# Kernel tuning notes

Hardware: AMD Instinct MI355X
Metric: run time of the kernel (lower is better)

## Reference

```python
import jax, jax.numpy as jnp
import numpy as np

N_NODES = 100000
N_EDGES = 800000
D_IN = 512
D_OUT = 512


def setup_inputs() -> dict:
    key = jax.random.key(0)
    ks = jax.random.split(key, 6)
    std = 1.0 / np.sqrt(D_OUT)
    return {
        "x": jax.random.normal(ks[0], (N_NODES, D_IN), dtype=jnp.float32),
        "adj_row": jax.random.randint(ks[1], (N_EDGES,), 0, N_NODES, dtype=jnp.int32),
        "adj_col": jax.random.randint(ks[2], (N_EDGES,), 0, N_NODES, dtype=jnp.int32),
        "adj_vals": jax.random.uniform(ks[3], (N_EDGES,), dtype=jnp.float32),
        "weight": jax.random.uniform(ks[4], (D_IN, D_OUT), minval=-std, maxval=std, dtype=jnp.float32),
        "b": jax.random.uniform(ks[5], (D_OUT,), minval=-std, maxval=std, dtype=jnp.float32),
    }


def reference(x, adj_row, adj_col, adj_vals, weight, b):
    # support = X W  : dense GEMM [N, D_in] x [D_in, D_out]
    support = jnp.matmul(x, weight)
    # output = A @ support + b, A given as COO (row, col, vals)
    gathered = adj_vals[:, None] * support[adj_col]  # [E, D_out]
    out = jax.ops.segment_sum(gathered, adj_row, num_segments=N_NODES)
    return out + b
```

## Files before the change

### kernel.cpp

```cpp
#include <hip/hip_runtime.h>
#include <hip/hip_bf16.h>
#include <stdint.h>

#define D 512
#define D4 (D / 4)

typedef __bf16 bf16x8 __attribute__((ext_vector_type(8)));
typedef float  f32x4  __attribute__((ext_vector_type(4)));

__device__ __forceinline__ unsigned short f2bf(float f) {
    uint32_t u = __float_as_uint(f);
    uint32_t r = u + 0x7fffu + ((u >> 16) & 1u);
    return (unsigned short)(r >> 16);
}

__device__ __forceinline__ uint32_t pack2(float lo, float hi) {
    return (uint32_t)f2bf(lo) | ((uint32_t)f2bf(hi) << 16);
}

__global__ __launch_bounds__(256) void cvt_x_kernel(const float4* __restrict__ x,
                                                    uint4* __restrict__ xb,
                                                    long n8) {
    long i = (long)blockIdx.x * 256 + threadIdx.x;
    if (i >= n8) return;
    float4 a = x[i * 2];
    float4 b = x[i * 2 + 1];
    uint4 o;
    o.x = pack2(a.x, a.y);
    o.y = pack2(a.z, a.w);
    o.z = pack2(b.x, b.y);
    o.w = pack2(b.z, b.w);
    xb[i] = o;
}

__global__ __launch_bounds__(256) void cvt_w_kernel(const float* __restrict__ w,
                                                    unsigned short* __restrict__ wt) {
    __shared__ float t[32][33];
    const int tx = threadIdx.x & 31;
    const int ty = threadIdx.x >> 5;
    const int n0 = blockIdx.x * 32;
    const int k0 = blockIdx.y * 32;
#pragma unroll
    for (int i = 0; i < 4; ++i)
        t[ty + i * 8][tx] = w[(long)(k0 + ty + i * 8) * D + n0 + tx];
    __syncthreads();
#pragma unroll
    for (int i = 0; i < 4; ++i)
        wt[(long)(n0 + ty + i * 8) * D + k0 + tx] = f2bf(t[tx][ty + i * 8]);
}

__global__ __launch_bounds__(256) void zero_kernel(int* __restrict__ p, int n) {
    int i = blockIdx.x * 256 + threadIdx.x;
    if (i < n) p[i] = 0;
}

__global__ __launch_bounds__(256) void hist_kernel(const int* __restrict__ erow,
                                                   int* __restrict__ cnt, int nE) {
    int i = blockIdx.x * 256 + threadIdx.x;
    int stride = gridDim.x * 256;
    for (; i < nE; i += stride) atomicAdd(&cnt[erow[i]], 1);
}

__global__ __launch_bounds__(1024) void scan_kernel(const int* __restrict__ cnt,
                                                    int* __restrict__ rowptr,
                                                    int* __restrict__ heads,
                                                    int M) {
    __shared__ int wsum[16];
    __shared__ int wpre[16];
    __shared__ int s_carry;
    const int lane = threadIdx.x & 63;
    const int wv   = threadIdx.x >> 6;
    if (threadIdx.x == 0) s_carry = 0;
    __syncthreads();
    for (int base = 0; base < M; base += 1024) {
        const int i = base + (int)threadIdx.x;
        const int v = (i < M) ? cnt[i] : 0;
        int s = v;
#pragma unroll
        for (int off = 1; off < 64; off <<= 1) {
            int t = __shfl_up(s, off);
            if (lane >= off) s += t;
        }
        if (lane == 63) wsum[wv] = s;
        __syncthreads();
        if (threadIdx.x == 0) {
            int acc = s_carry;
#pragma unroll
            for (int j = 0; j < 16; ++j) { wpre[j] = acc; acc += wsum[j]; }
            s_carry = acc;
        }
        __syncthreads();
        const int excl = wpre[wv] + s - v;
        if (i < M) { rowptr[i] = excl; heads[i] = excl; }
        __syncthreads();
    }
    if (threadIdx.x == 0) rowptr[M] = s_carry;
}

__global__ __launch_bounds__(256) void edge_sort_kernel(const int* __restrict__ erow,
                                                        const int* __restrict__ ecol,
                                                        const float* __restrict__ eval,
                                                        int* __restrict__ heads,
                                                        int* __restrict__ scol,
                                                        float* __restrict__ sval,
                                                        int nE) {
    int i = blockIdx.x * 256 + threadIdx.x;
    int stride = gridDim.x * 256;
    for (; i < nE; i += stride) {
        const int r = erow[i];
        const int p = atomicAdd(&heads[r], 1);
        scol[p] = ecol[i];
        sval[p] = eval[i];
    }
}

__global__ __launch_bounds__(256) void gemm_kernel(const unsigned short* __restrict__ Xb,
                                                   const unsigned short* __restrict__ Wt,
                                                   unsigned short* __restrict__ Sup,
                                                   int M) {
    __shared__ __align__(16) unsigned short As[128 * 64];
    __shared__ __align__(16) unsigned short Bs[128 * 64];
    const int tid  = threadIdx.x;
    const int wv   = tid >> 6;
    const int lane = tid & 63;
    const int tileM = blockIdx.x * 128;
    const int tileN = blockIdx.y * 128;
    const int wm = wv >> 1, wn = wv & 1;

    f32x4 acc[4][4];
#pragma unroll
    for (int i = 0; i < 4; ++i)
#pragma unroll
        for (int j = 0; j < 4; ++j) acc[i][j] = (f32x4)0.0f;

    const int srow = lane >> 3;
    const int sgrn = (lane & 7) ^ srow;
    const int scol = sgrn * 8;

    const int fm  = lane & 15;
    const int fkq = lane >> 4;

    for (int kt = 0; kt < D; kt += 64) {
        __syncthreads();
#pragma unroll
        for (int i = 0; i < 4; ++i) {
            const int c   = wv * 4 + i;
            const int row = c * 8 + srow;
            int rg = tileM + row;
            rg = (rg < M) ? rg : (M - 1);
            const unsigned short* ga = Xb + (long)rg * D + kt + scol;
            __builtin_amdgcn_global_load_lds(
                (const __attribute__((address_space(1))) void*)ga,
                (__attribute__((address_space(3))) void*)(As + c * 512), 16, 0, 0);
            const unsigned short* gb = Wt + (long)(tileN + row) * D + kt + scol;
            __builtin_amdgcn_global_load_lds(
                (const __attribute__((address_space(1))) void*)gb,
                (__attribute__((address_space(3))) void*)(Bs + c * 512), 16, 0, 0);
        }
        __syncthreads();
#pragma unroll
        for (int kk = 0; kk < 2; ++kk) {
            bf16x8 af[4], bfr[4];
#pragma unroll
            for (int mi = 0; mi < 4; ++mi) {
                const int m = wm * 64 + mi * 16 + fm;
                const int g = (kk * 4 + fkq) ^ (m & 7);
                af[mi] = *(const bf16x8*)(As + m * 64 + g * 8);
            }
#pragma unroll
            for (int ni = 0; ni < 4; ++ni) {
                const int n = wn * 64 + ni * 16 + fm;
                const int g = (kk * 4 + fkq) ^ (n & 7);
                bfr[ni] = *(const bf16x8*)(Bs + n * 64 + g * 8);
            }
#pragma unroll
            for (int mi = 0; mi < 4; ++mi)
#pragma unroll
                for (int ni = 0; ni < 4; ++ni)
                    acc[mi][ni] = __builtin_amdgcn_mfma_f32_16x16x32_bf16(
                        af[mi], bfr[ni], acc[mi][ni], 0, 0, 0);
        }
    }

    const int colb = tileN + wn * 64 + fm;
#pragma unroll
    for (int mi = 0; mi < 4; ++mi) {
        const int rb = tileM + wm * 64 + mi * 16 + fkq * 4;
#pragma unroll
        for (int r = 0; r < 4; ++r) {
            const int row = rb + r;
            if (row < M) {
                unsigned short* dst = Sup + (long)row * D + colb;
#pragma unroll
                for (int ni = 0; ni < 4; ++ni)
                    dst[ni * 16] = f2bf(acc[mi][ni][r]);
            }
        }
    }
}

__global__ __launch_bounds__(256) void aggregate_kernel(const unsigned short* __restrict__ sup,
                                                        const int* __restrict__ rowptr,
                                                        const int* __restrict__ scol,
                                                        const float* __restrict__ sval,
                                                        const float* __restrict__ bias,
                                                        float* __restrict__ out,
                                                        int M) {
    const int lane = threadIdx.x & 63;
    const int row  = (int)((blockIdx.x * 256 + threadIdx.x) >> 6);
    if (row >= M) return;
    const int beg = rowptr[row];
    const int end = rowptr[row + 1];

    const float4 b0 = ((const float4*)bias)[lane * 2];
    const float4 b1 = ((const float4*)bias)[lane * 2 + 1];
    float acc[8] = {b0.x, b0.y, b0.z, b0.w, b1.x, b1.y, b1.z, b1.w};

    for (int e = beg; e < end; ++e) {
        const int c   = scol[e];
        const float v = sval[e];
        const uint4 p = *(const uint4*)(sup + (long)c * D + lane * 8);
        const uint32_t pk[4] = {p.x, p.y, p.z, p.w};
#pragma unroll
        for (int i = 0; i < 4; ++i) {
            acc[i * 2]     += v * __uint_as_float((pk[i] & 0x0000ffffu) << 16);
            acc[i * 2 + 1] += v * __uint_as_float(pk[i] & 0xffff0000u);
        }
    }

    float4* dst = (float4*)(out + (long)row * D);
    dst[lane * 2]     = (float4){acc[0], acc[1], acc[2], acc[3]};
    dst[lane * 2 + 1] = (float4){acc[4], acc[5], acc[6], acc[7]};
}

extern "C" void kernel_launch(void* const* d_in, const int* in_sizes, int n_in,
                              void* d_out, int out_size, void* d_ws, size_t ws_size,
                              hipStream_t stream) {
    const float* x        = (const float*)d_in[0];
    const int*   adj_row  = (const int*)d_in[1];
    const int*   adj_col  = (const int*)d_in[2];
    const float* adj_vals = (const float*)d_in[3];
    const float* weight   = (const float*)d_in[4];
    const float* bias     = (const float*)d_in[5];
    float* out = (float*)d_out;

    const int M = in_sizes[0] / D;
    const int E = in_sizes[1];

    char* ws = (char*)d_ws;
    size_t off = 0;
    unsigned short* Xb  = (unsigned short*)(ws + off); off += (size_t)M * D * 2;
    unsigned short* Sup = (unsigned short*)(ws + off); off += (size_t)M * D * 2;
    unsigned short* Wt  = (unsigned short*)(ws + off); off += (size_t)D * D * 2;
    int*   rowptr = (int*)(ws + off);   off += (size_t)(M + 1) * 4;
    int*   heads  = (int*)(ws + off);   off += (size_t)M * 4;
    int*   scol   = (int*)(ws + off);   off += (size_t)E * 4;
    float* sval   = (float*)(ws + off); off += (size_t)E * 4;
    int* cnt = heads;

    zero_kernel<<<(M + 255) / 256, 256, 0, stream>>>(cnt, M);
    hist_kernel<<<1024, 256, 0, stream>>>(adj_row, cnt, E);
    scan_kernel<<<1, 1024, 0, stream>>>(cnt, rowptr, heads, M);
    edge_sort_kernel<<<1024, 256, 0, stream>>>(adj_row, adj_col, adj_vals,
                                               heads, scol, sval, E);

    {
        long n8 = (long)M * D / 8;
        cvt_x_kernel<<<(int)((n8 + 255) / 256), 256, 0, stream>>>(
            (const float4*)x, (uint4*)Xb, n8);
    }
    cvt_w_kernel<<<dim3(D / 32, D / 32), 256, 0, stream>>>(weight, Wt);
    gemm_kernel<<<dim3((M + 127) / 128, D / 128), 256, 0, stream>>>(Xb, Wt, Sup, M);

    aggregate_kernel<<<(M * 64 + 255) / 256, 256, 0, stream>>>(
        Sup, rowptr, scol, sval, bias, out, M);
}
```

Baseline: 723.2 us.

## Parallelize row-pointer scan across blocks and unroll aggregate gather loop

Replaces the single-block sequential prefix scan over node counts with a three-phase multi-block scan: per-block partial sums, a one-block scan of those sums, then per-block final scans. The aggregate kernel's edge loop is unrolled by four and two so several gathered support rows are in flight at once. Output rows are written with nontemporal stores. The scan change removes a serial bottleneck at the cost of two extra launches, and the unrolling raises register pressure.

```diff
diff --git a/kernel.cpp b/kernel.cpp
--- a/kernel.cpp
+++ b/kernel.cpp
@@ -4,6 +4,7 @@
 
 #define D 512
 #define D4 (D / 4)
+#define SB 256
 
 typedef __bf16 bf16x8 __attribute__((ext_vector_type(8)));
 typedef float  f32x4  __attribute__((ext_vector_type(4)));
@@ -61,20 +62,62 @@
     for (; i < nE; i += stride) atomicAdd(&cnt[erow[i]], 1);
 }
 
-__global__ __launch_bounds__(1024) void scan_kernel(const int* __restrict__ cnt,
-                                                    int* __restrict__ rowptr,
-                                                    int* __restrict__ heads,
-                                                    int M) {
-    __shared__ int wsum[16];
-    __shared__ int wpre[16];
-    __shared__ int s_carry;
+__global__ __launch_bounds__(256) void scan_part_kernel(const int* __restrict__ cnt,
+                                                        int* __restrict__ bsum, int M) {
+    const int b = blockIdx.x;
+    const int chunk = (M + SB - 1) / SB;
+    const int lo = b * chunk;
+    const int hi = min(M, lo + chunk);
+    int s = 0;
+    for (int i = lo + (int)threadIdx.x; i < hi; i += 256) s += cnt[i];
+#pragma unroll
+    for (int off = 32; off; off >>= 1) s += __shfl_down(s, off);
+    __shared__ int ws[4];
+    const int wv = threadIdx.x >> 6;
+    if ((threadIdx.x & 63) == 0) ws[wv] = s;
+    __syncthreads();
+    if (threadIdx.x == 0) bsum[b] = ws[0] + ws[1] + ws[2] + ws[3];
+}
+
+__global__ __launch_bounds__(SB) void scan_base_kernel(const int* __restrict__ bsum,
+                                                       int* __restrict__ bbase,
+                                                       int* __restrict__ rowptr, int M) {
+    const int tid  = (int)threadIdx.x;
+    const int lane = tid & 63;
+    const int wv   = tid >> 6;
+    const int v = bsum[tid];
+    int s = v;
+#pragma unroll
+    for (int off = 1; off < 64; off <<= 1) {
+        int t = __shfl_up(s, off);
+        if (lane >= off) s += t;
+    }
+    __shared__ int wsum[4];
+    if (lane == 63) wsum[wv] = s;
+    __syncthreads();
+    int wb = 0;
+    for (int j = 0; j < wv; ++j) wb += wsum[j];
+    bbase[tid] = wb + s - v;
+    if (tid == SB - 1) rowptr[M] = wb + s;
+}
+
+__global__ __launch_bounds__(256) void scan_final_kernel(const int* __restrict__ cnt,
+                                                         const int* __restrict__ bbase,
+                                                         int* __restrict__ rowptr,
+                                                         int* __restrict__ heads, int M) {
+    const int b = blockIdx.x;
+    const int chunk = (M + SB - 1) / SB;
+    const int lo = b * chunk;
+    const int hi = min(M, lo + chunk);
     const int lane = threadIdx.x & 63;
     const int wv   = threadIdx.x >> 6;
-    if (threadIdx.x == 0) s_carry = 0;
+    __shared__ int wsum[4];
+    __shared__ int s_carry;
+    if (threadIdx.x == 0) s_carry = bbase[b];
     __syncthreads();
-    for (int base = 0; base < M; base += 1024) {
+    for (int base = lo; base < hi; base += 256) {
         const int i = base + (int)threadIdx.x;
-        const int v = (i < M) ? cnt[i] : 0;
+        const int v = (i < hi) ? cnt[i] : 0;
         int s = v;
 #pragma unroll
         for (int off = 1; off < 64; off <<= 1) {
@@ -83,18 +126,14 @@
         }
         if (lane == 63) wsum[wv] = s;
         __syncthreads();
-        if (threadIdx.x == 0) {
-            int acc = s_carry;
-#pragma unroll
-            for (int j = 0; j < 16; ++j) { wpre[j] = acc; acc += wsum[j]; }
-            s_carry = acc;
-        }
-        __syncthreads();
-        const int excl = wpre[wv] + s - v;
-        if (i < M) { rowptr[i] = excl; heads[i] = excl; }
-        __syncthreads();
-    }
-    if (threadIdx.x == 0) rowptr[M] = s_carry;
+        int wb = s_carry;
+        for (int j = 0; j < wv; ++j) wb += wsum[j];
+        const int excl = wb + s - v;
+        if (i < hi) { rowptr[i] = excl; heads[i] = excl; }
+        __syncthreads();
+        if (threadIdx.x == 0) s_carry += wsum[0] + wsum[1] + wsum[2] + wsum[3];
+        __syncthreads();
+    }
 }
 
 __global__ __launch_bounds__(256) void edge_sort_kernel(const int* __restrict__ erow,
@@ -209,14 +248,54 @@
     const int lane = threadIdx.x & 63;
     const int row  = (int)((blockIdx.x * 256 + threadIdx.x) >> 6);
     if (row >= M) return;
-    const int beg = rowptr[row];
+    int e = rowptr[row];
     const int end = rowptr[row + 1];
 
     const float4 b0 = ((const float4*)bias)[lane * 2];
     const float4 b1 = ((const float4*)bias)[lane * 2 + 1];
     float acc[8] = {b0.x, b0.y, b0.z, b0.w, b1.x, b1.y, b1.z, b1.w};
 
-    for (int e = beg; e < end; ++e) {
+    for (; e + 4 <= end; e += 4) {
+        const int c0 = scol[e + 0], c1 = scol[e + 1];
+        const int c2 = scol[e + 2], c3 = scol[e + 3];
+        const float v0 = sval[e + 0], v1 = sval[e + 1];
+        const float v2 = sval[e + 2], v3 = sval[e + 3];
+        const uint4 p0 = *(const uint4*)(sup + (long)c0 * D + lane * 8);
+        const uint4 p1 = *(const uint4*)(sup + (long)c1 * D + lane * 8);
+        const uint4 p2 = *(const uint4*)(sup + (long)c2 * D + lane * 8);
+        const uint4 p3 = *(const uint4*)(sup + (long)c3 * D + lane * 8);
+        const uint32_t pk0[4] = {p0.x, p0.y, p0.z, p0.w};
+        const uint32_t pk1[4] = {p1.x, p1.y, p1.z, p1.w};
+        const uint32_t pk2[4] = {p2.x, p2.y, p2.z, p2.w};
+        const uint32_t pk3[4] = {p3.x, p3.y, p3.z, p3.w};
+#pragma unroll
+        for (int i = 0; i < 4; ++i) {
+            acc[i * 2]     += v0 * __uint_as_float((pk0[i] & 0x0000ffffu) << 16);
+            acc[i * 2 + 1] += v0 * __uint_as_float(pk0[i] & 0xffff0000u);
+            acc[i * 2]     += v1 * __uint_as_float((pk1[i] & 0x0000ffffu) << 16);
+            acc[i * 2 + 1] += v1 * __uint_as_float(pk1[i] & 0xffff0000u);
+            acc[i * 2]     += v2 * __uint_as_float((pk2[i] & 0x0000ffffu) << 16);
+            acc[i * 2 + 1] += v2 * __uint_as_float(pk2[i] & 0xffff0000u);
+            acc[i * 2]     += v3 * __uint_as_float((pk3[i] & 0x0000ffffu) << 16);
+            acc[i * 2 + 1] += v3 * __uint_as_float(pk3[i] & 0xffff0000u);
+        }
+    }
+    for (; e + 2 <= end; e += 2) {
+        const int c0 = scol[e + 0], c1 = scol[e + 1];
+        const float v0 = sval[e + 0], v1 = sval[e + 1];
+        const uint4 p0 = *(const uint4*)(sup + (long)c0 * D + lane * 8);
+        const uint4 p1 = *(const uint4*)(sup + (long)c1 * D + lane * 8);
+        const uint32_t pk0[4] = {p0.x, p0.y, p0.z, p0.w};
+        const uint32_t pk1[4] = {p1.x, p1.y, p1.z, p1.w};
+#pragma unroll
+        for (int i = 0; i < 4; ++i) {
+            acc[i * 2]     += v0 * __uint_as_float((pk0[i] & 0x0000ffffu) << 16);
+            acc[i * 2 + 1] += v0 * __uint_as_float(pk0[i] & 0xffff0000u);
+            acc[i * 2]     += v1 * __uint_as_float((pk1[i] & 0x0000ffffu) << 16);
+            acc[i * 2 + 1] += v1 * __uint_as_float(pk1[i] & 0xffff0000u);
+        }
+    }
+    for (; e < end; ++e) {
         const int c   = scol[e];
         const float v = sval[e];
         const uint4 p = *(const uint4*)(sup + (long)c * D + lane * 8);
@@ -228,9 +307,11 @@
         }
     }
 
-    float4* dst = (float4*)(out + (long)row * D);
-    dst[lane * 2]     = (float4){acc[0], acc[1], acc[2], acc[3]};
-    dst[lane * 2 + 1] = (float4){acc[4], acc[5], acc[6], acc[7]};
+    f32x4* dst = (f32x4*)(out + (long)row * D);
+    f32x4 o0 = {acc[0], acc[1], acc[2], acc[3]};
+    f32x4 o1 = {acc[4], acc[5], acc[6], acc[7]};
+    __builtin_nontemporal_store(o0, dst + lane * 2);
+    __builtin_nontemporal_store(o1, dst + lane * 2 + 1);
 }
 
 extern "C" void kernel_launch(void* const* d_in, const int* in_sizes, int n_in,
@@ -256,11 +337,15 @@
     int*   heads  = (int*)(ws + off);   off += (size_t)M * 4;
     int*   scol   = (int*)(ws + off);   off += (size_t)E * 4;
     float* sval   = (float*)(ws + off); off += (size_t)E * 4;
+    int*   bsum   = (int*)(ws + off);   off += (size_t)SB * 4;
+    int*   bbase  = (int*)(ws + off);   off += (size_t)SB * 4;
     int* cnt = heads;
 
     zero_kernel<<<(M + 255) / 256, 256, 0, stream>>>(cnt, M);
     hist_kernel<<<1024, 256, 0, stream>>>(adj_row, cnt, E);
-    scan_kernel<<<1, 1024, 0, stream>>>(cnt, rowptr, heads, M);
+    scan_part_kernel<<<SB, 256, 0, stream>>>(cnt, bsum, M);
+    scan_base_kernel<<<1, SB, 0, stream>>>(bsum, bbase, rowptr, M);
+    scan_final_kernel<<<SB, 256, 0, stream>>>(cnt, bbase, rowptr, heads, M);
     edge_sort_kernel<<<1024, 256, 0, stream>>>(adj_row, adj_col, adj_vals,
                                                heads, scol, sval, E);
 
```

After: 656.8 us. 9.2% less time.
